# Performance work log

Hardware: AMD Instinct MI355X
Metric: run time of the kernel (lower is better)

## Reference

```python
import jax, jax.numpy as jnp
import numpy as np

N_NODES, N_EDGES, DIM, N_GRAPHS = 200000, 400000, 256, 2048


def _mlp_params(key, dim):
    # MLP([dim, dim//2, dim//4, 1]) -> 3 Linear layers
    k1, k2, k3 = jax.random.split(key, 3)
    def lin(k, fi, fo):
        s = 1.0 / np.sqrt(fi)
        kw, kb = jax.random.split(k)
        W = jax.random.uniform(kw, (fi, fo), jnp.float32, -s, s)
        b = jax.random.uniform(kb, (fo,), jnp.float32, -s, s)
        return W, b
    W1, b1 = lin(k1, dim, dim // 2)
    W2, b2 = lin(k2, dim // 2, dim // 4)
    W3, b3 = lin(k3, dim // 4, 1)
    return W1, b1, W2, b2, W3, b3


def setup_inputs() -> dict:
    key = jax.random.key(0)
    kn, ke, kin, kie, kpn, kpe = jax.random.split(key, 6)
    emb_nodes = jax.random.normal(kn, (N_NODES, DIM), jnp.float32)
    emb_edges = jax.random.normal(ke, (N_EDGES, DIM), jnp.float32)
    node_index = jnp.sort(jax.random.randint(kin, (N_NODES,), 0, N_GRAPHS, jnp.int32))
    edge_index = jnp.sort(jax.random.randint(kie, (N_EDGES,), 0, N_GRAPHS, jnp.int32))
    Wn1, bn1, Wn2, bn2, Wn3, bn3 = _mlp_params(kpn, DIM)
    We1, be1, We2, be2, We3, be3 = _mlp_params(kpe, DIM)
    return {
        "emb_nodes": emb_nodes, "emb_edges": emb_edges,
        "node_index": node_index, "edge_index": edge_index,
        "Wn1": Wn1, "bn1": bn1, "Wn2": Wn2, "bn2": bn2, "Wn3": Wn3, "bn3": bn3,
        "We1": We1, "be1": be1, "We2": We2, "be2": be2, "We3": We3, "be3": be3,
        "num_graphs": N_GRAPHS,
    }


def _gated_att_pool(src, index, W1, b1, W2, b2, W3, b3, num_segments):
    # att MLP: dim -> dim/2 -> dim/4 -> 1 (ReLU between hidden layers)
    h = jax.nn.relu(src @ W1 + b1)
    h = jax.nn.relu(h @ W2 + b2)
    logits = (h @ W3 + b3).reshape(-1)  # [N]
    # scatter_softmax over segments (numerically stable)
    m = jax.ops.segment_max(logits, index, num_segments=num_segments)
    e = jnp.exp(logits - m[index])
    s = jax.ops.segment_sum(e, index, num_segments=num_segments)
    att = (e / s[index])[:, None]  # [N,1]
    # weighted scatter_add -> [num_segments, dim]
    return jax.ops.segment_sum(att * src, index, num_segments=num_segments)


def reference(emb_nodes, emb_edges, node_index, edge_index,
              Wn1, bn1, Wn2, bn2, Wn3, bn3,
              We1, be1, We2, be2, We3, be3, num_graphs):
    nodes_pooled = _gated_att_pool(emb_nodes, node_index, Wn1, bn1, Wn2, bn2, Wn3, bn3, num_graphs)
    edges_pooled = _gated_att_pool(emb_edges, edge_index, We1, be1, We2, be2, We3, be3, num_graphs)
    return nodes_pooled, edges_pooled
```

## Files before the change

### kernel.cpp

```cpp
#include <hip/hip_runtime.h>

typedef unsigned short ushort_t;
typedef __attribute__((ext_vector_type(8))) short short8;
typedef __attribute__((ext_vector_type(4))) float f32x4;

__device__ __forceinline__ ushort_t f2bf(float f) {
    union { float f; unsigned int u; } c; c.f = f;
    unsigned int r = c.u + 0x7fffu + ((c.u >> 16) & 1u);
    return (ushort_t)(r >> 16);
}

__global__ __launch_bounds__(256) void build_wfrags(
    const float* __restrict__ W1, const float* __restrict__ W2,
    ushort_t* __restrict__ W1f, ushort_t* __restrict__ W2f)
{
    int tid = blockIdx.x * 256 + threadIdx.x;
    if (tid < 32768) {
        int j = tid & 7, l = (tid >> 3) & 63, fi = tid >> 9;
        int nt = fi >> 3, kt = fi & 7;
        int n = nt * 16 + (l & 15);
        int k = kt * 32 + (l >> 4) * 8 + j;
        W1f[tid] = f2bf(W1[k * 128 + n]);
    } else if (tid < 40960) {
        int u = tid - 32768;
        int j = u & 7, l = (u >> 3) & 63, fi = u >> 9;
        int nt = fi >> 2, kt = fi & 3;
        int n = nt * 16 + (l & 15);
        int k = kt * 32 + (l >> 4) * 8 + j;
        W2f[u] = f2bf(W2[k * 64 + n]);
    }
}

#define MLP_WAVES 8
#define MLP_LDS_BYTES (32768 + MLP_WAVES * 16 * 136 * 2)

__global__ __launch_bounds__(512, 4) void mlp_logits_both(
    const float* __restrict__ Xn, const float* __restrict__ Xe,
    const ushort_t* __restrict__ W1f_n, const ushort_t* __restrict__ W2f_n,
    const ushort_t* __restrict__ W1f_e, const ushort_t* __restrict__ W2f_e,
    const float* __restrict__ bn1, const float* __restrict__ bn2,
    const float* __restrict__ Wn3, const float* __restrict__ bn3,
    const float* __restrict__ be1, const float* __restrict__ be2,
    const float* __restrict__ We3, const float* __restrict__ be3,
    float* __restrict__ log_n, float* __restrict__ log_e,
    int nsub_n, int nsub_e)
{
    extern __shared__ __align__(16) char smem[];
    ushort_t* h1base = (ushort_t*)(smem + 32768);

    const int t = threadIdx.x;
    const int w = t >> 6, lane = t & 63;
    const int q = lane >> 4, c16 = lane & 15;

    {
        const f32x4* sn = (const f32x4*)W2f_n; f32x4* dn = (f32x4*)smem;
        for (int i = t; i < 1024; i += 512) dn[i] = sn[i];
        const f32x4* se = (const f32x4*)W2f_e; f32x4* de = (f32x4*)(smem + 16384);
        for (int i = t; i < 1024; i += 512) de[i] = se[i];
    }
    __syncthreads();

    const int s_glob = blockIdx.x * MLP_WAVES + w;
    if (s_glob >= nsub_n + nsub_e) return;
    const bool is_e = (s_glob >= nsub_n);
    const int s = is_e ? (s_glob - nsub_n) : s_glob;

    const float*    X      = is_e ? Xe : Xn;
    const ushort_t* W1f    = is_e ? W1f_e : W1f_n;
    const ushort_t* W2s    = (ushort_t*)(is_e ? (smem + 16384) : smem);
    const float*    b1     = is_e ? be1 : bn1;
    const float*    b2     = is_e ? be2 : bn2;
    const float*    W3     = is_e ? We3 : Wn3;
    const float*    b3     = is_e ? be3 : bn3;
    float*          logits = is_e ? log_e : log_n;

    float bias1[8], bias2[4], w3v[4];
    #pragma unroll
    for (int nt = 0; nt < 8; ++nt) bias1[nt] = b1[nt * 16 + c16];
    #pragma unroll
    for (int nt = 0; nt < 4; ++nt) bias2[nt] = b2[nt * 16 + c16];
    #pragma unroll
    for (int nt = 0; nt < 4; ++nt) w3v[nt] = W3[nt * 16 + c16];
    const float b3v = b3[0];

    ushort_t* hw = h1base + w * (16 * 136);

    const float* xp = X + (size_t)(s * 16 + c16) * 256 + q * 8;

    f32x4 acc[8];
    #pragma unroll
    for (int nt = 0; nt < 8; ++nt) acc[nt] = (f32x4){0.f, 0.f, 0.f, 0.f};
    #pragma unroll
    for (int kt = 0; kt < 8; ++kt) {
        f32x4 x0 = *(const f32x4*)(xp + kt * 32);
        f32x4 x1 = *(const f32x4*)(xp + kt * 32 + 4);
        short8 a;
        #pragma unroll
        for (int j = 0; j < 4; ++j) {
            a[j]     = (short)f2bf(x0[j]);
            a[4 + j] = (short)f2bf(x1[j]);
        }
        #pragma unroll
        for (int nt = 0; nt < 8; ++nt) {
            short8 bf = *(const short8*)(W1f + ((nt * 8 + kt) * 64 + lane) * 8);
            acc[nt] = __builtin_amdgcn_mfma_f32_16x16x32_bf16(a, bf, acc[nt], 0, 0, 0);
        }
    }

    #pragma unroll
    for (int nt = 0; nt < 8; ++nt)
        #pragma unroll
        for (int reg = 0; reg < 4; ++reg)
            hw[(q * 4 + reg) * 136 + nt * 16 + c16] =
                f2bf(fmaxf(acc[nt][reg] + bias1[nt], 0.f));

    f32x4 acc2[4];
    #pragma unroll
    for (int nt = 0; nt < 4; ++nt) acc2[nt] = (f32x4){0.f, 0.f, 0.f, 0.f};
    #pragma unroll
    for (int kt = 0; kt < 4; ++kt) {
        short8 a = *(const short8*)(hw + c16 * 136 + kt * 32 + q * 8);
        #pragma unroll
        for (int nt = 0; nt < 4; ++nt) {
            short8 bf = *(const short8*)(W2s + ((nt * 4 + kt) * 64 + lane) * 8);
            acc2[nt] = __builtin_amdgcn_mfma_f32_16x16x32_bf16(a, bf, acc2[nt], 0, 0, 0);
        }
    }

    float p[4];
    #pragma unroll
    for (int reg = 0; reg < 4; ++reg) {
        float v = 0.f;
        #pragma unroll
        for (int nt = 0; nt < 4; ++nt)
            v += fmaxf(acc2[nt][reg] + bias2[nt], 0.f) * w3v[nt];
        p[reg] = v;
    }
    #pragma unroll
    for (int msk = 1; msk < 16; msk <<= 1)
        #pragma unroll
        for (int reg = 0; reg < 4; ++reg)
            p[reg] += __shfl_xor(p[reg], msk);
    if (c16 == 0) {
        #pragma unroll
        for (int reg = 0; reg < 4; ++reg)
            logits[s * 16 + q * 4 + reg] = p[reg] + b3v;
    }
}

__global__ __launch_bounds__(256) void pool_both(
    const float* __restrict__ Xn, const float* __restrict__ Xe,
    const int* __restrict__ idxn, const int* __restrict__ idxe,
    const float* __restrict__ log_n, const float* __restrict__ log_e,
    float* __restrict__ out)
{
    const int gb = blockIdx.x;
    const bool is_e = (gb >= 2048);
    const int g = is_e ? gb - 2048 : gb;
    const float* X      = is_e ? Xe : Xn;
    const int*   idx    = is_e ? idxe : idxn;
    const float* logits = is_e ? log_e : log_n;
    const int    nrows  = is_e ? 400000 : 200000;

    const int t = threadIdx.x;
    const int w = t >> 6, lane = t & 63;

    int lo = 0, hi = nrows;
    while (lo < hi) { int mid = (lo + hi) >> 1; if (idx[mid] < g) lo = mid + 1; else hi = mid; }
    const int start = lo;
    hi = nrows;
    while (lo < hi) { int mid = (lo + hi) >> 1; if (idx[mid] < g + 1) lo = mid + 1; else hi = mid; }
    const int cnt = lo - start;

    __shared__ float red[8];
    __shared__ float parts[4][256];

    const float* lg = logits + start;

    float m = -3.0e38f;
    for (int i = t; i < cnt; i += 256) m = fmaxf(m, lg[i]);
    #pragma unroll
    for (int o = 32; o; o >>= 1) m = fmaxf(m, __shfl_xor(m, o));
    if (lane == 0) red[w] = m;
    __syncthreads();
    m = fmaxf(fmaxf(red[0], red[1]), fmaxf(red[2], red[3]));

    float ssum = 0.f;
    for (int i = t; i < cnt; i += 256) ssum += __expf(lg[i] - m);
    #pragma unroll
    for (int o = 32; o; o >>= 1) ssum += __shfl_xor(ssum, o);
    if (lane == 0) red[4 + w] = ssum;
    __syncthreads();
    ssum = red[4] + red[5] + red[6] + red[7];
    const float inv = (cnt > 0) ? 1.f / ssum : 0.f;

    f32x4 acc = {0.f, 0.f, 0.f, 0.f};
    const float* xb = X + (size_t)start * 256 + lane * 4;
    int r = w;
    for (; r + 12 < cnt; r += 16) {
        float a0 = __expf(lg[r] - m);
        float a1 = __expf(lg[r + 4] - m);
        float a2 = __expf(lg[r + 8] - m);
        float a3 = __expf(lg[r + 12] - m);
        f32x4 x0 = *(const f32x4*)(xb + (size_t)(r) * 256);
        f32x4 x1 = *(const f32x4*)(xb + (size_t)(r + 4) * 256);
        f32x4 x2 = *(const f32x4*)(xb + (size_t)(r + 8) * 256);
        f32x4 x3 = *(const f32x4*)(xb + (size_t)(r + 12) * 256);
        acc += a0 * x0;
        acc += a1 * x1;
        acc += a2 * x2;
        acc += a3 * x3;
    }
    for (; r < cnt; r += 4) {
        float a = __expf(lg[r] - m);
        f32x4 xv = *(const f32x4*)(xb + (size_t)r * 256);
        acc += a * xv;
    }
    #pragma unroll
    for (int j = 0; j < 4; ++j) parts[w][lane * 4 + j] = acc[j] * inv;
    __syncthreads();
    out[(size_t)gb * 256 + t] = parts[0][t] + parts[1][t] + parts[2][t] + parts[3][t];
}


extern "C" void kernel_launch(void* const* d_in, const int* in_sizes, int n_in,
                              void* d_out, int out_size, void* d_ws, size_t ws_size,
                              hipStream_t stream) {
    const float* Xn  = (const float*)d_in[0];
    const float* Xe  = (const float*)d_in[1];
    const int* idxn  = (const int*)d_in[2];
    const int* idxe  = (const int*)d_in[3];
    const float* Wn1 = (const float*)d_in[4];
    const float* bn1 = (const float*)d_in[5];
    const float* Wn2 = (const float*)d_in[6];
    const float* bn2 = (const float*)d_in[7];
    const float* Wn3 = (const float*)d_in[8];
    const float* bn3 = (const float*)d_in[9];
    const float* We1 = (const float*)d_in[10];
    const float* be1 = (const float*)d_in[11];
    const float* We2 = (const float*)d_in[12];
    const float* be2 = (const float*)d_in[13];
    const float* We3 = (const float*)d_in[14];
    const float* be3 = (const float*)d_in[15];
    float* out = (float*)d_out;

    char* ws = (char*)d_ws;
    ushort_t* W1f_n = (ushort_t*)(ws + 0);
    ushort_t* W2f_n = (ushort_t*)(ws + 65536);
    ushort_t* W1f_e = (ushort_t*)(ws + 81920);
    ushort_t* W2f_e = (ushort_t*)(ws + 147456);
    float* log_n = (float*)(ws + 163840);
    float* log_e = (float*)(ws + 963840);

    (void)hipFuncSetAttribute((const void*)mlp_logits_both,
                              hipFuncAttributeMaxDynamicSharedMemorySize,
                              MLP_LDS_BYTES);

    build_wfrags<<<160, 256, 0, stream>>>(Wn1, Wn2, W1f_n, W2f_n);
    build_wfrags<<<160, 256, 0, stream>>>(We1, We2, W1f_e, W2f_e);

    const int nsub_n = 200000 / 16, nsub_e = 400000 / 16;
    const int nblk = (nsub_n + nsub_e + MLP_WAVES - 1) / MLP_WAVES;
    mlp_logits_both<<<nblk, 512, MLP_LDS_BYTES, stream>>>(
        Xn, Xe, W1f_n, W2f_n, W1f_e, W2f_e,
        bn1, bn2, Wn3, bn3, be1, be2, We3, be3,
        log_n, log_e, nsub_n, nsub_e);

    pool_both<<<4096, 256, 0, stream>>>(Xn, Xe, idxn, idxe, log_n, log_e, out);
}
```

Before: 863.7 us.

## Stage W1 fragments in LDS and prefetch all X loads per wave

Each block now handles only one of the two inputs (nodes or edges), so it copies that input's full 64KB W1 fragment set plus its W2 set into LDS instead of both W2 sets. The layer-1 MFMA loop then reads B fragments from LDS instead of global memory. All 16 X vectors per lane are loaded up front to raise memory-level parallelism. In exchange, each block spends time loading 80KB of weights and the larger LDS footprint (about 115KB) allows only one 512-thread block per CU. The min-blocks launch bound was also dropped, which frees more registers for the prefetch.

```diff
diff --git a/kernel.cpp b/kernel.cpp
--- a/kernel.cpp
+++ b/kernel.cpp
@@ -32,9 +32,9 @@
 }
 
 #define MLP_WAVES 8
-#define MLP_LDS_BYTES (32768 + MLP_WAVES * 16 * 136 * 2)
-
-__global__ __launch_bounds__(512, 4) void mlp_logits_both(
+#define MLP_LDS_BYTES (65536 + 16384 + MLP_WAVES * 16 * 136 * 2)
+
+__global__ __launch_bounds__(512) void mlp_logits_both(
     const float* __restrict__ Xn, const float* __restrict__ Xe,
     const ushort_t* __restrict__ W1f_n, const ushort_t* __restrict__ W2f_n,
     const ushort_t* __restrict__ W1f_e, const ushort_t* __restrict__ W2f_e,
@@ -43,36 +43,38 @@
     const float* __restrict__ be1, const float* __restrict__ be2,
     const float* __restrict__ We3, const float* __restrict__ be3,
     float* __restrict__ log_n, float* __restrict__ log_e,
-    int nsub_n, int nsub_e)
+    int nsub_n, int nsub_e, int nblk_n)
 {
     extern __shared__ __align__(16) char smem[];
-    ushort_t* h1base = (ushort_t*)(smem + 32768);
+    ushort_t* W1s    = (ushort_t*)smem;
+    ushort_t* W2s    = (ushort_t*)(smem + 65536);
+    ushort_t* h1base = (ushort_t*)(smem + 81920);
 
     const int t = threadIdx.x;
     const int w = t >> 6, lane = t & 63;
     const int q = lane >> 4, c16 = lane & 15;
 
-    {
-        const f32x4* sn = (const f32x4*)W2f_n; f32x4* dn = (f32x4*)smem;
-        for (int i = t; i < 1024; i += 512) dn[i] = sn[i];
-        const f32x4* se = (const f32x4*)W2f_e; f32x4* de = (f32x4*)(smem + 16384);
-        for (int i = t; i < 1024; i += 512) de[i] = se[i];
-    }
-    __syncthreads();
-
-    const int s_glob = blockIdx.x * MLP_WAVES + w;
-    if (s_glob >= nsub_n + nsub_e) return;
-    const bool is_e = (s_glob >= nsub_n);
-    const int s = is_e ? (s_glob - nsub_n) : s_glob;
-
+    const bool is_e = (int)blockIdx.x >= nblk_n;
     const float*    X      = is_e ? Xe : Xn;
     const ushort_t* W1f    = is_e ? W1f_e : W1f_n;
-    const ushort_t* W2s    = (ushort_t*)(is_e ? (smem + 16384) : smem);
+    const ushort_t* W2f    = is_e ? W2f_e : W2f_n;
     const float*    b1     = is_e ? be1 : bn1;
     const float*    b2     = is_e ? be2 : bn2;
     const float*    W3     = is_e ? We3 : Wn3;
     const float*    b3     = is_e ? be3 : bn3;
     float*          logits = is_e ? log_e : log_n;
+    const int       nsub   = is_e ? nsub_e : nsub_n;
+
+    {
+        const f32x4* s1 = (const f32x4*)W1f; f32x4* d1 = (f32x4*)W1s;
+        for (int i = t; i < 4096; i += 512) d1[i] = s1[i];
+        const f32x4* s2 = (const f32x4*)W2f; f32x4* d2 = (f32x4*)W2s;
+        for (int i = t; i < 1024; i += 512) d2[i] = s2[i];
+    }
+    __syncthreads();
+
+    const int s = (is_e ? (int)blockIdx.x - nblk_n : (int)blockIdx.x) * MLP_WAVES + w;
+    if (s >= nsub) return;
 
     float bias1[8], bias2[4], w3v[4];
     #pragma unroll
@@ -87,22 +89,27 @@
 
     const float* xp = X + (size_t)(s * 16 + c16) * 256 + q * 8;
 
+    f32x4 xv[16];
+    #pragma unroll
+    for (int kt = 0; kt < 8; ++kt) {
+        xv[2 * kt]     = *(const f32x4*)(xp + kt * 32);
+        xv[2 * kt + 1] = *(const f32x4*)(xp + kt * 32 + 4);
+    }
+
     f32x4 acc[8];
     #pragma unroll
     for (int nt = 0; nt < 8; ++nt) acc[nt] = (f32x4){0.f, 0.f, 0.f, 0.f};
     #pragma unroll
     for (int kt = 0; kt < 8; ++kt) {
-        f32x4 x0 = *(const f32x4*)(xp + kt * 32);
-        f32x4 x1 = *(const f32x4*)(xp + kt * 32 + 4);
         short8 a;
         #pragma unroll
         for (int j = 0; j < 4; ++j) {
-            a[j]     = (short)f2bf(x0[j]);
-            a[4 + j] = (short)f2bf(x1[j]);
+            a[j]     = (short)f2bf(xv[2 * kt][j]);
+            a[4 + j] = (short)f2bf(xv[2 * kt + 1][j]);
         }
         #pragma unroll
         for (int nt = 0; nt < 8; ++nt) {
-            short8 bf = *(const short8*)(W1f + ((nt * 8 + kt) * 64 + lane) * 8);
+            short8 bf = *(const short8*)(W1s + ((nt * 8 + kt) * 64 + lane) * 8);
             acc[nt] = __builtin_amdgcn_mfma_f32_16x16x32_bf16(a, bf, acc[nt], 0, 0, 0);
         }
     }
@@ -260,11 +267,12 @@
     build_wfrags<<<160, 256, 0, stream>>>(We1, We2, W1f_e, W2f_e);
 
     const int nsub_n = 200000 / 16, nsub_e = 400000 / 16;
-    const int nblk = (nsub_n + nsub_e + MLP_WAVES - 1) / MLP_WAVES;
-    mlp_logits_both<<<nblk, 512, MLP_LDS_BYTES, stream>>>(
+    const int nblk_n = (nsub_n + MLP_WAVES - 1) / MLP_WAVES;
+    const int nblk_e = (nsub_e + MLP_WAVES - 1) / MLP_WAVES;
+    mlp_logits_both<<<nblk_n + nblk_e, 512, MLP_LDS_BYTES, stream>>>(
         Xn, Xe, W1f_n, W2f_n, W1f_e, W2f_e,
         bn1, bn2, Wn3, bn3, be1, be2, We3, be3,
-        log_n, log_e, nsub_n, nsub_e);
+        log_n, log_e, nsub_n, nsub_e, nblk_n);
 
     pool_both<<<4096, 256, 0, stream>>>(Xn, Xe, idxn, idxe, log_n, log_e, out);
 }
```

After: 832.1 us. -3.7%, faster.
